# Kernel tuning notes

Hardware: AMD Instinct MI355X
Metric: run time of the kernel (lower is better)

The kernel has to match this reference:

```python
import jax, jax.numpy as jnp
import numpy as np

B, T, C = 64, 256, 384
H = 6
D = C // H  # head_size = 64


def setup_inputs() -> dict:
    key = jax.random.key(0)
    ks = jax.random.split(key, 6)
    s = 1.0 / np.sqrt(C)
    return {
        "x": jax.random.normal(ks[0], (B, T, C), dtype=jnp.float32),
        "Wk": jax.random.uniform(ks[1], (C, C), jnp.float32, -s, s),
        "Wq": jax.random.uniform(ks[2], (C, C), jnp.float32, -s, s),
        "Wv": jax.random.uniform(ks[3], (C, C), jnp.float32, -s, s),
        "Wo": jax.random.uniform(ks[4], (C, C), jnp.float32, -s, s),
        "bo": jax.random.uniform(ks[5], (C,), jnp.float32, -s, s),
    }


def reference(x, Wk, Wq, Wv, Wo, bo):
    b, t, c = x.shape
    # QKV projections (no bias), split heads: [B, H, T, D]
    k = (x @ Wk.T).reshape(b, t, H, D).transpose(0, 2, 1, 3)
    q = (x @ Wq.T).reshape(b, t, H, D).transpose(0, 2, 1, 3)
    v = (x @ Wv.T).reshape(b, t, H, D).transpose(0, 2, 1, 3)
    # Scores scaled by C**-0.5 (as in the original module, not head_size**-0.5)
    wei = jnp.einsum("bhqd,bhkd->bhqk", q, k) * (c ** -0.5)
    mask = jnp.tril(jnp.ones((t, t), dtype=bool))
    wei = jnp.where(mask, wei, -jnp.inf)
    wei = jax.nn.softmax(wei, axis=-1)
    out = jnp.einsum("bhqk,bhkd->bhqd", wei, v)
    out = out.transpose(0, 2, 1, 3).reshape(b, t, c)
    # Output projection (dropout is identity at inference)
    return out @ Wo.T + bo
```

## Files before the change

kernel.cpp:

```cpp
#include <hip/hip_runtime.h>
#include <hip/hip_bf16.h>

typedef unsigned short u16;
typedef __attribute__((ext_vector_type(8))) short short8;
typedef __attribute__((ext_vector_type(4))) float f32x4;

#define BATCH 64
#define SEQ   256
#define CDIM  384
#define NHEAD 6
#define DHEAD 64
#define NROW  16384

constexpr float SCALE = 0.051031036307982884f;

__device__ __forceinline__ f32x4 mfma16(short8 a, short8 b, f32x4 c) {
    return __builtin_amdgcn_mfma_f32_16x16x32_bf16(a, b, c, 0, 0, 0);
}

__device__ __forceinline__ u16 f2b(float f) {
    __hip_bfloat16 h = __float2bfloat16(f);
    return *reinterpret_cast<u16*>(&h);
}

__device__ __forceinline__ void gload_lds16(const u16* g, u16* l) {
    __builtin_amdgcn_global_load_lds(
        (const __attribute__((address_space(1))) void*)g,
        (__attribute__((address_space(3))) void*)l, 16, 0, 0);
}

__global__ __launch_bounds__(256) void cvt_all(
        const float* __restrict__ x,
        const float* __restrict__ Wk, const float* __restrict__ Wq,
        const float* __restrict__ Wv, const float* __restrict__ Wo,
        u16* __restrict__ xb,
        u16* __restrict__ wkb, u16* __restrict__ wqb,
        u16* __restrict__ wvb, u16* __restrict__ wob)
{
    int blk = blockIdx.x;
    const float* s;
    u16* d;
    if (blk < 3072) {
        s = x; d = xb;
    } else {
        const int w = blk - 3072;
        const int z = w / 72;
        blk = w - z * 72;
        s = (z == 0) ? Wk : (z == 1) ? Wq : (z == 2) ? Wv : Wo;
        d = (z == 0) ? wkb : (z == 1) ? wqb : (z == 2) ? wvb : wob;
    }
    const int i = (blk * 256 + (int)threadIdx.x) * 8;
    const float4 a = *(const float4*)(s + i);
    const float4 b = *(const float4*)(s + i + 4);
    short8 r;
    r[0] = (short)f2b(a.x); r[1] = (short)f2b(a.y);
    r[2] = (short)f2b(a.z); r[3] = (short)f2b(a.w);
    r[4] = (short)f2b(b.x); r[5] = (short)f2b(b.y);
    r[6] = (short)f2b(b.z); r[7] = (short)f2b(b.w);
    *(short8*)(d + i) = r;
}

__global__ __launch_bounds__(256) void gemm_qkv(
        const u16* __restrict__ X, const u16* __restrict__ Wk,
        const u16* __restrict__ Wv, const u16* __restrict__ Wq,
        u16* __restrict__ Kd, u16* __restrict__ VTd, u16* __restrict__ Qd)
{
    __shared__ u16 SMEM[17408];
    u16* As = SMEM;
    u16* Bs = SMEM + 8192;

    const int bid   = blockIdx.x;
    const int xcd   = bid & 7;
    const int i     = bid >> 3;
    const int igrp  = i / 9;
    const int j     = i - igrp * 9;
    const int panel = xcd * 16 + igrp;
    const int m0    = panel * 128;
    const int n0    = (j % 3) * 128;
    const int z     = j / 3;
    const u16* W = (z == 0) ? Wk : (z == 1 ? Wv : Wq);

    const int tid  = threadIdx.x;
    const int lane = tid & 63;
    const int wv   = tid >> 6;
    const int l15  = lane & 15;
    const int q4   = lane >> 4;
    const int wm   = (wv >> 1) * 64;
    const int wn   = (wv & 1) * 64;

    f32x4 acc[4][4] = {};

    for (int kk = 0; kk < CDIM; kk += 64) {
        __syncthreads();
#pragma unroll
        for (int ch = 0; ch < 4; ++ch) {
            const int f = (ch * 256 + tid) * 8;
            const int r = f >> 6;
            const int c = (f ^ ((r & 7) << 3)) & 63;
            const int lb = (ch * 256 + wv * 64) * 8;
            gload_lds16(X + (size_t)(m0 + r) * CDIM + kk + c, As + lb);
            gload_lds16(W + (size_t)(n0 + r) * CDIM + kk + c, Bs + lb);
        }
        __syncthreads();

#pragma unroll
        for (int ks = 0; ks < 2; ++ks) {
            short8 af[4], bf[4];
#pragma unroll
            for (int t = 0; t < 4; ++t) {
                const int ra = wm + t * 16 + l15;
                const int rb = wn + t * 16 + l15;
                af[t] = *(const short8*)(As + ra * 64 +
                        ((ks * 32 + q4 * 8) ^ ((ra & 7) << 3)));
                bf[t] = *(const short8*)(Bs + rb * 64 +
                        ((ks * 32 + q4 * 8) ^ ((rb & 7) << 3)));
            }
#pragma unroll
            for (int tm = 0; tm < 4; ++tm)
#pragma unroll
                for (int tn = 0; tn < 4; ++tn)
                    acc[tm][tn] = mfma16(af[tm], bf[tn], acc[tm][tn]);
        }
    }
    __syncthreads();

    if (z != 1) {
        u16* D = (z == 0) ? Kd : Qd;
        u16* T = SMEM;
#pragma unroll
        for (int tm = 0; tm < 4; ++tm)
#pragma unroll
            for (int tn = 0; tn < 4; ++tn) {
                const int cl = wn + tn * 16 + l15;
#pragma unroll
                for (int r = 0; r < 4; ++r) {
                    const int row = wm + tm * 16 + q4 * 4 + r;
                    T[row * 128 + (((cl >> 3) ^ (row & 7)) << 3) + (cl & 7)] =
                        f2b(acc[tm][tn][r]);
                }
            }
        __syncthreads();
        const int seg0 = tid >> 3;
        const int c    = tid & 7;
#pragma unroll
        for (int it = 0; it < 8; ++it) {
            const int S   = it * 32 + seg0;
            const int row = S >> 1;
            const int hf  = S & 1;
            const int rowg = m0 + row;
            const int b  = rowg >> 8, tt = rowg & 255;
            const int h  = (n0 + hf * 64) >> 6;
            const int chunk = (hf * 8 + c) ^ (row & 7);
            *(uint4*)(D + (size_t)((b * NHEAD + h) * SEQ + tt) * DHEAD + c * 8) =
                *(const uint4*)(T + row * 128 + chunk * 8);
        }
    } else {
        u16* T = SMEM;
#pragma unroll
        for (int tm = 0; tm < 4; ++tm)
#pragma unroll
            for (int tn = 0; tn < 4; ++tn) {
                const int cl = wn + tn * 16 + l15;
#pragma unroll
                for (int r = 0; r < 4; ++r) {
                    const int rl = wm + tm * 16 + q4 * 4 + r;
                    T[cl * 136 + rl] = f2b(acc[tm][tn][r]);
                }
            }
        __syncthreads();
        const int b  = m0 >> 8;
        const int t0 = m0 & 255;
        const int fl = tid >> 1;
        const int hf = tid & 1;
        const int fg = n0 + fl;
        const int h  = fg >> 6, d = fg & 63;
        u16* dst = VTd + ((size_t)(b * NHEAD + h) * DHEAD + d) * SEQ + t0 + hf * 64;
        const u16* src = T + fl * 136 + hf * 64;
#pragma unroll
        for (int j2 = 0; j2 < 8; ++j2)
            *(uint4*)(dst + j2 * 8) = *(const uint4*)(src + j2 * 8);
    }
}

#define PLD 264

template <int CH>
__device__ __forceinline__ void attn_body(
        const u16* __restrict__ Qg, const u16* __restrict__ Kg,
        const u16* __restrict__ VTg, u16* __restrict__ Og, int bh,
        u16* SA, u16* Pbase)
{
    constexpr int NKEY = 64 * (CH + 1);
    constexpr int KT   = NKEY / 16;
    constexpr int NPH  = (NKEY + 127) / 128;

    const int tid  = threadIdx.x;
    const int wv   = tid >> 6;
    const int lane = tid & 63;
    const int l15  = lane & 15;
    const int q4   = lane >> 4;
    const int qrow0 = CH * 64 + wv * 16;
    const int qmax  = qrow0 + 15;
    u16* Pl = Pbase + wv * 16 * PLD;

    short8 aq[2];
#pragma unroll
    for (int ks = 0; ks < 2; ++ks)
        aq[ks] = *(const short8*)(Qg + (size_t)(bh * SEQ + qrow0 + l15) * DHEAD
                                     + ks * 32 + q4 * 8);

    u16* Kbuf = SA;
    f32x4 s[KT];
#pragma unroll
    for (int ph = 0; ph < NPH; ++ph) {
        const int rows = (NKEY - ph * 128) < 128 ? (NKEY - ph * 128) : 128;
        for (int it = 0; it < rows / 32; ++it) {
            const int r  = it * 32 + (tid >> 3);
            const int d0 = (tid & 7) * 8;
            *(uint4*)(Kbuf + r * 72 + d0) =
                *(const uint4*)(Kg + (size_t)(bh * SEQ + ph * 128 + r) * DHEAD + d0);
        }
        __syncthreads();
#pragma unroll
        for (int t = 0; t < rows / 16; ++t) {
            const int gt = ph * 8 + t;
            if (gt * 16 <= qmax) {
                f32x4 z = {0.f, 0.f, 0.f, 0.f};
#pragma unroll
                for (int ks = 0; ks < 2; ++ks) {
                    short8 bk = *(const short8*)(Kbuf + (t * 16 + l15) * 72
                                                 + ks * 32 + q4 * 8);
                    z = mfma16(aq[ks], bk, z);
                }
                const int kc = gt * 16 + l15;
#pragma unroll
                for (int r = 0; r < 4; ++r) {
                    float v = z[r] * SCALE;
                    if (kc > qrow0 + q4 * 4 + r) v = -1e30f;
                    z[r] = v;
                }
                s[gt] = z;
            } else {
                f32x4 neg = {-1e30f, -1e30f, -1e30f, -1e30f};
                s[gt] = neg;
            }
        }
        __syncthreads();
    }

    float mx[4], sm[4], rs[4];
#pragma unroll
    for (int r = 0; r < 4; ++r) {
        float m = -1e30f;
#pragma unroll
        for (int t = 0; t < KT; ++t) m = fmaxf(m, s[t][r]);
#pragma unroll
        for (int off = 1; off < 16; off <<= 1)
            m = fmaxf(m, __shfl_xor(m, off, 16));
        mx[r] = m;
        sm[r] = 0.f;
    }
#pragma unroll
    for (int t = 0; t < KT; ++t)
#pragma unroll
        for (int r = 0; r < 4; ++r) {
            float p = __expf(s[t][r] - mx[r]);
            s[t][r] = p;
            sm[r] += p;
        }
#pragma unroll
    for (int r = 0; r < 4; ++r) {
#pragma unroll
        for (int off = 1; off < 16; off <<= 1)
            sm[r] += __shfl_xor(sm[r], off, 16);
        rs[r] = 1.f / sm[r];
    }

#pragma unroll
    for (int gt = 0; gt < KT; ++gt)
#pragma unroll
        for (int r = 0; r < 4; ++r)
            Pl[(q4 * 4 + r) * PLD + gt * 16 + l15] = f2b(s[gt][r]);

    u16* Vt = SA;
    f32x4 o[4] = {};
#pragma unroll
    for (int ph = 0; ph < NPH; ++ph) {
        const int rows = (NKEY - ph * 128) < 128 ? (NKEY - ph * 128) : 128;
        const int cpr  = rows >> 3;
#pragma unroll
        for (int it = 0; it < 4; ++it) {
            if (it < cpr / 4) {
                const int flat = it * 256 + tid;
                const int rd = flat / cpr;
                const int kc = (flat - rd * cpr) * 8;
                *(uint4*)(Vt + rd * 136 + kc) =
                    *(const uint4*)(VTg + ((size_t)bh * DHEAD + rd) * SEQ
                                        + ph * 128 + kc);
            }
        }
        __syncthreads();
#pragma unroll
        for (int ks = 0; ks < rows / 32; ++ks) {
            const int gks = ph * 4 + ks;
            if (gks * 32 <= qmax) {
                short8 ap = *(const short8*)(Pl + l15 * PLD + gks * 32 + q4 * 8);
#pragma unroll
                for (int tn = 0; tn < 4; ++tn) {
                    short8 bv = *(const short8*)(Vt + (tn * 16 + l15) * 136
                                                 + ks * 32 + q4 * 8);
                    o[tn] = mfma16(ap, bv, o[tn]);
                }
            }
        }
        __syncthreads();
    }

    u16* OL = SA;
#pragma unroll
    for (int tn = 0; tn < 4; ++tn) {
        const int col = tn * 16 + l15;
#pragma unroll
        for (int r = 0; r < 4; ++r) {
            const int row = wv * 16 + q4 * 4 + r;
            OL[row * 64 + (((col >> 3) ^ (row & 7)) << 3) + (col & 7)] =
                f2b(o[tn][r] * rs[r]);
        }
    }
    __syncthreads();
    const int b  = bh / NHEAD;
    const int h  = bh - b * NHEAD;
    const int seg0 = tid >> 3;
    const int c    = tid & 7;
#pragma unroll
    for (int it = 0; it < 2; ++it) {
        const int row = it * 32 + seg0;
        const int chunk = c ^ (row & 7);
        *(uint4*)(Og + (size_t)(b * SEQ + CH * 64 + row) * CDIM
                     + h * DHEAD + c * 8) =
            *(const uint4*)(OL + row * 64 + chunk * 8);
    }
}

__global__ __launch_bounds__(256) void attn_kernel(
        const u16* __restrict__ Qg, const u16* __restrict__ Kg,
        const u16* __restrict__ VTg, u16* __restrict__ Og)
{
    __shared__ u16 SA[128 * 72];
    __shared__ u16 Pls[4 * 16 * PLD];
    const int bh = blockIdx.y;
    switch (blockIdx.x) {
        case 0: attn_body<0>(Qg, Kg, VTg, Og, bh, SA, Pls); break;
        case 1: attn_body<1>(Qg, Kg, VTg, Og, bh, SA, Pls); break;
        case 2: attn_body<2>(Qg, Kg, VTg, Og, bh, SA, Pls); break;
        default: attn_body<3>(Qg, Kg, VTg, Og, bh, SA, Pls); break;
    }
}

__global__ __launch_bounds__(256) void gemm_out(
        const u16* __restrict__ O, const u16* __restrict__ Wo,
        const float* __restrict__ bias, float* __restrict__ out)
{
    __shared__ u16 As[64 * 64];
    __shared__ u16 Bs[128 * 64];

    const int n0 = blockIdx.x * 128;
    const int m0 = blockIdx.y * 64;

    const int tid  = threadIdx.x;
    const int lane = tid & 63;
    const int wv   = tid >> 6;
    const int l15  = lane & 15;
    const int q4   = lane >> 4;
    const int wm   = (wv >> 1) * 32;
    const int wn   = (wv & 1) * 64;

    f32x4 acc[2][4] = {};

    for (int kk = 0; kk < CDIM; kk += 64) {
        __syncthreads();
#pragma unroll
        for (int ch = 0; ch < 4; ++ch) {
            const int f = (ch * 256 + tid) * 8;
            const int r = f >> 6;
            const int c = (f ^ ((r & 7) << 3)) & 63;
            const int lb = (ch * 256 + wv * 64) * 8;
            gload_lds16(Wo + (size_t)(n0 + r) * CDIM + kk + c, Bs + lb);
            if (ch < 2)
                gload_lds16(O + (size_t)(m0 + r) * CDIM + kk + c, As + lb);
        }
        __syncthreads();

#pragma unroll
        for (int ks = 0; ks < 2; ++ks) {
            short8 af[2], bf[4];
#pragma unroll
            for (int t = 0; t < 2; ++t) {
                const int ra = wm + t * 16 + l15;
                af[t] = *(const short8*)(As + ra * 64 +
                        ((ks * 32 + q4 * 8) ^ ((ra & 7) << 3)));
            }
#pragma unroll
            for (int t = 0; t < 4; ++t) {
                const int rb = wn + t * 16 + l15;
                bf[t] = *(const short8*)(Bs + rb * 64 +
                        ((ks * 32 + q4 * 8) ^ ((rb & 7) << 3)));
            }
#pragma unroll
            for (int tm = 0; tm < 2; ++tm)
#pragma unroll
                for (int tn = 0; tn < 4; ++tn)
                    acc[tm][tn] = mfma16(af[tm], bf[tn], acc[tm][tn]);
        }
    }

#pragma unroll
    for (int tm = 0; tm < 2; ++tm) {
#pragma unroll
        for (int tn = 0; tn < 4; ++tn) {
            const int col = n0 + wn + tn * 16 + l15;
            const float bb = bias[col];
#pragma unroll
            for (int r = 0; r < 4; ++r) {
                const int row = m0 + wm + tm * 16 + q4 * 4 + r;
                out[(size_t)row * CDIM + col] = acc[tm][tn][r] + bb;
            }
        }
    }
}

extern "C" void kernel_launch(void* const* d_in, const int* in_sizes, int n_in,
                              void* d_out, int out_size, void* d_ws, size_t ws_size,
                              hipStream_t stream)
{
    const float* x  = (const float*)d_in[0];
    const float* Wk = (const float*)d_in[1];
    const float* Wq = (const float*)d_in[2];
    const float* Wv = (const float*)d_in[3];
    const float* Wo = (const float*)d_in[4];
    const float* bo = (const float*)d_in[5];
    float* out = (float*)d_out;

    const size_t SZ = (size_t)NROW * CDIM;
    const size_t WZ = (size_t)CDIM * CDIM;
    u16* xb  = (u16*)d_ws;
    u16* Wkb = xb  + SZ;
    u16* Wqb = Wkb + WZ;
    u16* Wvb = Wqb + WZ;
    u16* Wob = Wvb + WZ;
    u16* Kw  = Wob + WZ;
    u16* Qw  = Kw + SZ;
    u16* Ow  = Qw + SZ;
    u16* VTw = (u16*)d_out;

    cvt_all<<<dim3(3360), 256, 0, stream>>>(
        x, Wk, Wq, Wv, Wo, xb, Wkb, Wqb, Wvb, Wob);

    gemm_qkv<<<dim3(1152), 256, 0, stream>>>(xb, Wkb, Wvb, Wqb, Kw, VTw, Qw);

    dim3 g2(4, BATCH * NHEAD);
    attn_kernel<<<g2, 256, 0, stream>>>(Qw, Kw, VTw, Ow);

    dim3 g3(CDIM / 128, NROW / 64);
    gemm_out<<<g3, 256, 0, stream>>>(Ow, Wob, bo, out);
}
```

Before: 152.3 us.

## Fuse fp32-to-bf16 conversion of x into QKV GEMM and remap grids per XCD

Drops the separate conversion pass over x: the QKV GEMM now loads fp32 x directly, packs it to bf16 in registers and writes it swizzled into LDS, while the weights are still converted by a smaller kernel. This removes a full write and reread of the bf16 copy of x. The attention and output-GEMM launches switch to 1D grids whose block indices are remapped so that blocks sharing a head or row panel land on the same XCD, aiming for better L2 reuse. The trade-off is that x is now read as fp32 on every N-tile pass, three times per K, V and Q, with synchronous register loads in place of async global-to-LDS copies.

After: 157.4 us. 1.03x slower.

```diff
diff --git a/kernel.cpp b/kernel.cpp
--- a/kernel.cpp
+++ b/kernel.cpp
@@ -23,45 +23,39 @@
     return *reinterpret_cast<u16*>(&h);
 }
 
-__device__ __forceinline__ void gload_lds16(const u16* g, u16* l) {
-    __builtin_amdgcn_global_load_lds(
-        (const __attribute__((address_space(1))) void*)g,
-        (__attribute__((address_space(3))) void*)l, 16, 0, 0);
-}
-
-__global__ __launch_bounds__(256) void cvt_all(
-        const float* __restrict__ x,
-        const float* __restrict__ Wk, const float* __restrict__ Wq,
-        const float* __restrict__ Wv, const float* __restrict__ Wo,
-        u16* __restrict__ xb,
-        u16* __restrict__ wkb, u16* __restrict__ wqb,
-        u16* __restrict__ wvb, u16* __restrict__ wob)
-{
-    int blk = blockIdx.x;
-    const float* s;
-    u16* d;
-    if (blk < 3072) {
-        s = x; d = xb;
-    } else {
-        const int w = blk - 3072;
-        const int z = w / 72;
-        blk = w - z * 72;
-        s = (z == 0) ? Wk : (z == 1) ? Wq : (z == 2) ? Wv : Wo;
-        d = (z == 0) ? wkb : (z == 1) ? wqb : (z == 2) ? wvb : wob;
-    }
-    const int i = (blk * 256 + (int)threadIdx.x) * 8;
-    const float4 a = *(const float4*)(s + i);
-    const float4 b = *(const float4*)(s + i + 4);
+__device__ __forceinline__ short8 pack8(float4 a, float4 b) {
     short8 r;
     r[0] = (short)f2b(a.x); r[1] = (short)f2b(a.y);
     r[2] = (short)f2b(a.z); r[3] = (short)f2b(a.w);
     r[4] = (short)f2b(b.x); r[5] = (short)f2b(b.y);
     r[6] = (short)f2b(b.z); r[7] = (short)f2b(b.w);
-    *(short8*)(d + i) = r;
+    return r;
+}
+
+__device__ __forceinline__ void gload_lds16(const u16* g, u16* l) {
+    __builtin_amdgcn_global_load_lds(
+        (const __attribute__((address_space(1))) void*)g,
+        (__attribute__((address_space(3))) void*)l, 16, 0, 0);
+}
+
+__global__ __launch_bounds__(256) void cvt_w(
+        const float* __restrict__ Wk, const float* __restrict__ Wq,
+        const float* __restrict__ Wv, const float* __restrict__ Wo,
+        u16* __restrict__ wkb, u16* __restrict__ wqb,
+        u16* __restrict__ wvb, u16* __restrict__ wob)
+{
+    const int z   = blockIdx.x / 72;
+    const int blk = blockIdx.x - z * 72;
+    const float* s = (z == 0) ? Wk : (z == 1) ? Wq : (z == 2) ? Wv : Wo;
+    u16*         d = (z == 0) ? wkb : (z == 1) ? wqb : (z == 2) ? wvb : wob;
+    const int i = (blk * 256 + (int)threadIdx.x) * 8;
+    const float4 a = *(const float4*)(s + i);
+    const float4 b = *(const float4*)(s + i + 4);
+    *(short8*)(d + i) = pack8(a, b);
 }
 
 __global__ __launch_bounds__(256) void gemm_qkv(
-        const u16* __restrict__ X, const u16* __restrict__ Wk,
+        const float* __restrict__ X, const u16* __restrict__ Wk,
         const u16* __restrict__ Wv, const u16* __restrict__ Wq,
         u16* __restrict__ Kd, u16* __restrict__ VTd, u16* __restrict__ Qd)
 {
@@ -96,10 +90,14 @@
         for (int ch = 0; ch < 4; ++ch) {
             const int f = (ch * 256 + tid) * 8;
             const int r = f >> 6;
-            const int c = (f ^ ((r & 7) << 3)) & 63;
+            const int c = f & 63;
+            const int cb = (f ^ ((r & 7) << 3)) & 63;
             const int lb = (ch * 256 + wv * 64) * 8;
-            gload_lds16(X + (size_t)(m0 + r) * CDIM + kk + c, As + lb);
-            gload_lds16(W + (size_t)(n0 + r) * CDIM + kk + c, Bs + lb);
+            gload_lds16(W + (size_t)(n0 + r) * CDIM + kk + cb, Bs + lb);
+            const size_t gx = (size_t)(m0 + r) * CDIM + kk + c;
+            const float4 xa = *(const float4*)(X + gx);
+            const float4 xb = *(const float4*)(X + gx + 4);
+            *(short8*)(As + r * 64 + (c ^ ((r & 7) << 3))) = pack8(xa, xb);
         }
         __syncthreads();
 
@@ -348,8 +346,12 @@
 {
     __shared__ u16 SA[128 * 72];
     __shared__ u16 Pls[4 * 16 * PLD];
-    const int bh = blockIdx.y;
-    switch (blockIdx.x) {
+    const int bid = blockIdx.x;
+    const int xcd = bid & 7;
+    const int g   = bid >> 3;
+    const int bh  = xcd * 48 + (g >> 2);
+    const int ch  = g & 3;
+    switch (ch) {
         case 0: attn_body<0>(Qg, Kg, VTg, Og, bh, SA, Pls); break;
         case 1: attn_body<1>(Qg, Kg, VTg, Og, bh, SA, Pls); break;
         case 2: attn_body<2>(Qg, Kg, VTg, Og, bh, SA, Pls); break;
@@ -364,8 +366,12 @@
     __shared__ u16 As[64 * 64];
     __shared__ u16 Bs[128 * 64];
 
-    const int n0 = blockIdx.x * 128;
-    const int m0 = blockIdx.y * 64;
+    const int bid = blockIdx.x;
+    const int xcd = bid & 7;
+    const int g   = bid >> 3;
+    const int mt  = xcd * 32 + g / 3;
+    const int n0  = (g % 3) * 128;
+    const int m0  = mt * 64;
 
     const int tid  = threadIdx.x;
     const int lane = tid & 63;
@@ -443,8 +449,7 @@
 
     const size_t SZ = (size_t)NROW * CDIM;
     const size_t WZ = (size_t)CDIM * CDIM;
-    u16* xb  = (u16*)d_ws;
-    u16* Wkb = xb  + SZ;
+    u16* Wkb = (u16*)d_ws;
     u16* Wqb = Wkb + WZ;
     u16* Wvb = Wqb + WZ;
     u16* Wob = Wvb + WZ;
@@ -453,14 +458,12 @@
     u16* Ow  = Qw + SZ;
     u16* VTw = (u16*)d_out;
 
-    cvt_all<<<dim3(3360), 256, 0, stream>>>(
-        x, Wk, Wq, Wv, Wo, xb, Wkb, Wqb, Wvb, Wob);
-
-    gemm_qkv<<<dim3(1152), 256, 0, stream>>>(xb, Wkb, Wvb, Wqb, Kw, VTw, Qw);
-
-    dim3 g2(4, BATCH * NHEAD);
-    attn_kernel<<<g2, 256, 0, stream>>>(Qw, Kw, VTw, Ow);
-
-    dim3 g3(CDIM / 128, NROW / 64);
-    gemm_out<<<g3, 256, 0, stream>>>(Ow, Wob, bo, out);
-}
+    cvt_w<<<dim3(288), 256, 0, stream>>>(
+        Wk, Wq, Wv, Wo, Wkb, Wqb, Wvb, Wob);
+
+    gemm_qkv<<<dim3(1152), 256, 0, stream>>>(x, Wkb, Wvb, Wqb, Kw, VTw, Qw);
+
+    attn_kernel<<<dim3(1536), 256, 0, stream>>>(Qw, Kw, VTw, Ow);
+
+    gemm_out<<<dim3(768), 256, 0, stream>>>(Ow, Wob, bo, out);
+}
```

## Double-buffer QKV GEMM loads and remap attention/out-proj blocks per XCD

Applied to the files above, without the earlier changes.

The QKV GEMM now uses two LDS buffers. It prefetches the next K-slice with direct-to-LDS loads while the MFMAs run on the current one, using explicit vmcnt waits and raw barriers. This hides global load latency behind compute, and LDS use per block roughly doubles, which may reduce occupancy. The attention and output-projection kernels switch to 1D grids with XCD-aware block index remapping, so that blocks sharing the same head or row panel land on the same XCD and get better L2 locality.

Result: faster. 143.5 us (-5.8%).

```diff
diff --git a/kernel.cpp b/kernel.cpp
--- a/kernel.cpp
+++ b/kernel.cpp
@@ -65,9 +65,7 @@
         const u16* __restrict__ Wv, const u16* __restrict__ Wq,
         u16* __restrict__ Kd, u16* __restrict__ VTd, u16* __restrict__ Qd)
 {
-    __shared__ u16 SMEM[17408];
-    u16* As = SMEM;
-    u16* Bs = SMEM + 8192;
+    __shared__ u16 SMEM[32768];
 
     const int bid   = blockIdx.x;
     const int xcd   = bid & 7;
@@ -90,29 +88,42 @@
 
     f32x4 acc[4][4] = {};
 
-    for (int kk = 0; kk < CDIM; kk += 64) {
-        __syncthreads();
+    auto STAGE = [&](int kk, int buf) {
 #pragma unroll
         for (int ch = 0; ch < 4; ++ch) {
-            const int f = (ch * 256 + tid) * 8;
-            const int r = f >> 6;
-            const int c = (f ^ ((r & 7) << 3)) & 63;
-            const int lb = (ch * 256 + wv * 64) * 8;
-            gload_lds16(X + (size_t)(m0 + r) * CDIM + kk + c, As + lb);
-            gload_lds16(W + (size_t)(n0 + r) * CDIM + kk + c, Bs + lb);
-        }
-        __syncthreads();
-
+            const int f  = (ch * 256 + tid) * 8;
+            const int r  = f >> 6;
+            const int cb = (f ^ ((r & 7) << 3)) & 63;
+            const int lb = buf * 16384 + (ch * 256 + wv * 64) * 8;
+            gload_lds16(X + (size_t)(m0 + r) * CDIM + kk + cb, SMEM + lb);
+            gload_lds16(W + (size_t)(n0 + r) * CDIM + kk + cb, SMEM + 8192 + lb);
+        }
+    };
+
+    STAGE(0, 0);
+#pragma unroll
+    for (int t = 0; t < 6; ++t) {
+        const int cur = t & 1;
+        if (t < 5) {
+            STAGE((t + 1) * 64, cur ^ 1);
+            asm volatile("s_waitcnt vmcnt(8)" ::: "memory");
+        } else {
+            asm volatile("s_waitcnt vmcnt(0)" ::: "memory");
+        }
+        asm volatile("s_barrier" ::: "memory");
+
+        const u16* As = SMEM + cur * 16384;
+        const u16* Bs = SMEM + cur * 16384 + 8192;
 #pragma unroll
         for (int ks = 0; ks < 2; ++ks) {
             short8 af[4], bf[4];
 #pragma unroll
-            for (int t = 0; t < 4; ++t) {
-                const int ra = wm + t * 16 + l15;
-                const int rb = wn + t * 16 + l15;
-                af[t] = *(const short8*)(As + ra * 64 +
+            for (int tt = 0; tt < 4; ++tt) {
+                const int ra = wm + tt * 16 + l15;
+                const int rb = wn + tt * 16 + l15;
+                af[tt] = *(const short8*)(As + ra * 64 +
                         ((ks * 32 + q4 * 8) ^ ((ra & 7) << 3)));
-                bf[t] = *(const short8*)(Bs + rb * 64 +
+                bf[tt] = *(const short8*)(Bs + rb * 64 +
                         ((ks * 32 + q4 * 8) ^ ((rb & 7) << 3)));
             }
 #pragma unroll
@@ -121,8 +132,8 @@
                 for (int tn = 0; tn < 4; ++tn)
                     acc[tm][tn] = mfma16(af[tm], bf[tn], acc[tm][tn]);
         }
-    }
-    __syncthreads();
+        asm volatile("s_barrier" ::: "memory");
+    }
 
     if (z != 1) {
         u16* D = (z == 0) ? Kd : Qd;
@@ -348,8 +359,12 @@
 {
     __shared__ u16 SA[128 * 72];
     __shared__ u16 Pls[4 * 16 * PLD];
-    const int bh = blockIdx.y;
-    switch (blockIdx.x) {
+    const int bid = blockIdx.x;
+    const int xcd = bid & 7;
+    const int g   = bid >> 3;
+    const int bh  = xcd * 48 + (g >> 2);
+    const int ch  = g & 3;
+    switch (ch) {
         case 0: attn_body<0>(Qg, Kg, VTg, Og, bh, SA, Pls); break;
         case 1: attn_body<1>(Qg, Kg, VTg, Og, bh, SA, Pls); break;
         case 2: attn_body<2>(Qg, Kg, VTg, Og, bh, SA, Pls); break;
@@ -364,8 +379,12 @@
     __shared__ u16 As[64 * 64];
     __shared__ u16 Bs[128 * 64];
 
-    const int n0 = blockIdx.x * 128;
-    const int m0 = blockIdx.y * 64;
+    const int bid = blockIdx.x;
+    const int xcd = bid & 7;
+    const int g   = bid >> 3;
+    const int mt  = xcd * 32 + g / 3;
+    const int n0  = (g % 3) * 128;
+    const int m0  = mt * 64;
 
     const int tid  = threadIdx.x;
     const int lane = tid & 63;
@@ -458,9 +477,7 @@
 
     gemm_qkv<<<dim3(1152), 256, 0, stream>>>(xb, Wkb, Wvb, Wqb, Kw, VTw, Qw);
 
-    dim3 g2(4, BATCH * NHEAD);
-    attn_kernel<<<g2, 256, 0, stream>>>(Qw, Kw, VTw, Ow);
-
-    dim3 g3(CDIM / 128, NROW / 64);
-    gemm_out<<<g3, 256, 0, stream>>>(Ow, Wob, bo, out);
-}
+    attn_kernel<<<dim3(1536), 256, 0, stream>>>(Qw, Kw, VTw, Ow);
+
+    gemm_out<<<dim3(768), 256, 0, stream>>>(Ow, Wob, bo, out);
+}
```
